# Optimization experiments

Hardware: AMD Instinct MI355X
Metric: run time of the kernel (lower is better)

Reference implementation:

```python
import jax, jax.numpy as jnp
import numpy as np

B, A, C, H, S, NR = 128, 2048, 128, 512, 3, 2
PR = C + 3 + S   # 134 read params per head
PW = 3 * C + 3 + S  # 390 write params


def setup_inputs() -> dict:
    key = jax.random.key(0)
    ks = jax.random.split(key, 8)
    h = jax.random.normal(ks[0], (B, H), jnp.float32)
    mem = jax.random.normal(ks[1], (B, A, C), jnp.float32)
    ra = jax.random.uniform(ks[2], (NR, B, A), jnp.float32)
    ra = ra / ra.sum(-1, keepdims=True)  # valid attention distributions
    wa = jax.random.uniform(ks[3], (B, A), jnp.float32)
    wa = wa / wa.sum(-1, keepdims=True)
    W_read = 0.02 * jax.random.normal(ks[4], (NR, PR, H), jnp.float32)
    b_read = jnp.zeros((NR, PR), jnp.float32)
    W_write = 0.02 * jax.random.normal(ks[5], (PW, H), jnp.float32)
    b_write = jnp.zeros((PW,), jnp.float32)
    return dict(h=h, mem=mem, prev_read_attn=ra, prev_write_attn=wa,
                W_read=W_read, b_read=b_read, W_write=W_write, b_write=b_write)


def _addressing(query, beta, gate, shift, gamma, mem, prev_w):
    """NTM addressing. query [...,C] (raw), beta/gate/gamma [...,1], shift [...,S],
    mem [B,A,C] (broadcasts), prev_w [...,A]. Returns attention [...,A]."""
    eps = 1e-8
    q = jax.nn.sigmoid(query)
    beta = jax.nn.softplus(beta) + 1.0
    gate = jax.nn.sigmoid(gate)
    shift_w = jax.nn.softmax(shift, axis=-1)
    gamma = jax.nn.softplus(gamma) + 1.0
    # content-based addressing: cosine similarity + sharpened softmax over A
    qn = jnp.maximum(jnp.linalg.norm(q, axis=-1, keepdims=True), eps)      # [...,1]
    mn = jnp.maximum(jnp.linalg.norm(mem, axis=-1), eps)                   # [B,A]
    sim = jnp.einsum('...c,...ac->...a', q, mem) / (qn * mn)
    w_c = jax.nn.softmax(beta * sim, axis=-1)
    # gated interpolation with previous attention
    w_g = gate * w_c + (1.0 - gate) * prev_w
    # circular shift convolution, offsets -(S//2)..S//2
    K = S // 2
    idx = (jnp.arange(A)[:, None] - (jnp.arange(S)[None, :] - K)) % A      # [A,S]
    w_s = jnp.einsum('...as,...s->...a', w_g[..., idx], shift_w)
    # gamma sharpening
    w_pow = w_s ** gamma
    return w_pow / (w_pow.sum(-1, keepdims=True) + 1e-12)


def reference(h, mem, prev_read_attn, prev_write_attn, W_read, b_read, W_write, b_write):
    # --- read heads (vectorized over NR heads) ---
    pr = jnp.einsum('bh,rph->rbp', h, W_read) + b_read[:, None, :]         # [NR,B,PR]
    q, beta, gate, shift, gamma = jnp.split(pr, [C, C + 1, C + 2, C + 2 + S], axis=-1)
    read_w = _addressing(q, beta, gate, shift, gamma, mem, prev_read_attn)  # [NR,B,A]
    read_vectors = jnp.einsum('rba,bac->rbc', read_w, mem)                 # [NR,B,C]
    # --- write head ---
    pw = h @ W_write.T + b_write                                           # [B,PW]
    locs = np.cumsum([C, 1, 1, S, 1, C])
    qw, bw, gw, sw, gmw, erase, add = jnp.split(pw, locs.tolist(), axis=-1)
    write_w = _addressing(qw, bw, gw, sw, gmw, mem, prev_write_attn)       # [B,A]
    e = jax.nn.sigmoid(erase)[:, None, :]                                  # [B,1,C]
    a = jax.nn.sigmoid(add)[:, None, :]                                    # [B,1,C]
    w = write_w[..., None]                                                 # [B,A,1]
    new_mem = mem * (1.0 - w * e) + w * a
    return read_vectors, new_mem
```

## Files before the change

kernel.cpp:

```cpp
#include <hip/hip_runtime.h>
#include <math.h>

constexpr int B_  = 128;
constexpr int A_  = 2048;
constexpr int C_  = 128;
constexpr int H_  = 512;
constexpr int S_  = 3;
constexpr int NR_ = 2;
constexpr int PR_ = C_ + 3 + S_;
constexpr int PW_ = 3 * C_ + 3 + S_;

typedef float vfloat4 __attribute__((ext_vector_type(4)));

__device__ __forceinline__ float sigmoidf_(float x) { return 1.0f / (1.0f + expf(-x)); }
__device__ __forceinline__ float softplusf_(float x) {
  return fmaxf(x, 0.0f) + log1pf(expf(-fabsf(x)));
}

__device__ __forceinline__ float waveReduceSum(float v) {
#pragma unroll
  for (int off = 32; off; off >>= 1) v += __shfl_xor(v, off, 64);
  return v;
}
__device__ __forceinline__ float waveReduceMax(float v) {
#pragma unroll
  for (int off = 32; off; off >>= 1) v = fmaxf(v, __shfl_xor(v, off, 64));
  return v;
}

__global__ __launch_bounds__(256) void proj_kernel(
    const float* __restrict__ h, const float* __restrict__ Wr,
    const float* __restrict__ br, const float* __restrict__ Ww,
    const float* __restrict__ bw, float* __restrict__ pr, float* __restrict__ pw) {
  constexpr int NPR = NR_ * B_ * PR_;
  constexpr int NPW = B_ * PW_;
  int wave = (blockIdx.x * blockDim.x + threadIdx.x) >> 6;
  int lane = threadIdx.x & 63;
  int out0 = wave * 2;
  const float* w0row;
  const float* w1row;
  const float* hrow;
  float bias0, bias1;
  float* outp;
  if (out0 < NPR) {
    int r = out0 / (B_ * PR_);
    int rem = out0 - r * (B_ * PR_);
    int b = rem / PR_;
    int p = rem - b * PR_;
    w0row = Wr + (size_t)(r * PR_ + p) * H_;
    w1row = w0row + H_;
    hrow = h + (size_t)b * H_;
    bias0 = br[r * PR_ + p];
    bias1 = br[r * PR_ + p + 1];
    outp = pr + out0;
  } else {
    int w2 = out0 - NPR;
    if (w2 >= NPW) return;
    int b = w2 / PW_;
    int p = w2 - b * PW_;
    w0row = Ww + (size_t)p * H_;
    w1row = w0row + H_;
    hrow = h + (size_t)b * H_;
    bias0 = bw[p];
    bias1 = bw[p + 1];
    outp = pw + w2;
  }
  const float4* h4 = (const float4*)hrow;
  const float4* wa4 = (const float4*)w0row;
  const float4* wb4 = (const float4*)w1row;
  float4 a0 = h4[(lane << 1)];
  float4 a1 = h4[(lane << 1) + 1];
  float4 b0 = wa4[(lane << 1)];
  float4 b1 = wa4[(lane << 1) + 1];
  float4 c0 = wb4[(lane << 1)];
  float4 c1 = wb4[(lane << 1) + 1];
  float acc0 = a0.x * b0.x;
  acc0 = fmaf(a0.y, b0.y, acc0);
  acc0 = fmaf(a0.z, b0.z, acc0);
  acc0 = fmaf(a0.w, b0.w, acc0);
  acc0 = fmaf(a1.x, b1.x, acc0);
  acc0 = fmaf(a1.y, b1.y, acc0);
  acc0 = fmaf(a1.z, b1.z, acc0);
  acc0 = fmaf(a1.w, b1.w, acc0);
  float acc1 = a0.x * c0.x;
  acc1 = fmaf(a0.y, c0.y, acc1);
  acc1 = fmaf(a0.z, c0.z, acc1);
  acc1 = fmaf(a0.w, c0.w, acc1);
  acc1 = fmaf(a1.x, c1.x, acc1);
  acc1 = fmaf(a1.y, c1.y, acc1);
  acc1 = fmaf(a1.z, c1.z, acc1);
  acc1 = fmaf(a1.w, c1.w, acc1);
  acc0 = waveReduceSum(acc0);
  acc1 = waveReduceSum(acc1);
  if (lane == 0) {
    outp[0] = acc0 + bias0;
    outp[1] = acc1 + bias1;
  }
}

__global__ __launch_bounds__(1024) void mega_kernel(
    const float* __restrict__ mem, const float* __restrict__ ra,
    const float* __restrict__ wa, const float* __restrict__ pr,
    const float* __restrict__ pw, float* __restrict__ rv,
    float* __restrict__ nmem) {
  __shared__ float sims[3][A_];
  __shared__ float wg[A_];
  __shared__ __align__(16) float qs[3 * C_];
  __shared__ float iqn[3];
  __shared__ float rbuf[16];
  __shared__ float4 red[2][16][32];

  int b = blockIdx.x;
  int tid = threadIdx.x;
  int lane = tid & 63;
  int wv = tid >> 6;

  if (tid < 3 * C_) {
    int hd = tid >> 7;
    int c = tid & (C_ - 1);
    float raw = (hd < 2) ? pr[(size_t)(hd * B_ + b) * PR_ + c]
                         : pw[(size_t)b * PW_ + c];
    qs[tid] = sigmoidf_(raw);
  }
  __syncthreads();
  if (wv < 3) {
    float v0 = qs[wv * C_ + lane];
    float v1 = qs[wv * C_ + 64 + lane];
    float ss = v0 * v0 + v1 * v1;
    ss = waveReduceSum(ss);
    if (lane == 0) iqn[wv] = 1.0f / fmaxf(sqrtf(ss), 1e-8f);
  }
  __syncthreads();

  {
    int j = tid & 7;
    int rgrp = tid >> 3;
    float4 q0[4], q1[4], q2[4];
    const float4* qs4 = (const float4*)qs;
#pragma unroll
    for (int k = 0; k < 4; k++) {
      q0[k] = qs4[j + 8 * k];
      q1[k] = qs4[32 + j + 8 * k];
      q2[k] = qs4[64 + j + 8 * k];
    }
    float iq0 = iqn[0], iq1 = iqn[1], iq2 = iqn[2];
#pragma unroll 2
    for (int i = 0; i < 16; i++) {
      int row = (i << 7) + rgrp;
      const float4* mrow = (const float4*)(mem + ((size_t)b * A_ + row) * C_);
      float d0 = 0.f, d1 = 0.f, d2 = 0.f, ss = 0.f;
#pragma unroll
      for (int k = 0; k < 4; k++) {
        float4 m = mrow[j + 8 * k];
        d0 = fmaf(m.x, q0[k].x, d0); d0 = fmaf(m.y, q0[k].y, d0);
        d0 = fmaf(m.z, q0[k].z, d0); d0 = fmaf(m.w, q0[k].w, d0);
        d1 = fmaf(m.x, q1[k].x, d1); d1 = fmaf(m.y, q1[k].y, d1);
        d1 = fmaf(m.z, q1[k].z, d1); d1 = fmaf(m.w, q1[k].w, d1);
        d2 = fmaf(m.x, q2[k].x, d2); d2 = fmaf(m.y, q2[k].y, d2);
        d2 = fmaf(m.z, q2[k].z, d2); d2 = fmaf(m.w, q2[k].w, d2);
        ss = fmaf(m.x, m.x, ss); ss = fmaf(m.y, m.y, ss);
        ss = fmaf(m.z, m.z, ss); ss = fmaf(m.w, m.w, ss);
      }
#pragma unroll
      for (int off = 1; off <= 4; off <<= 1) {
        d0 += __shfl_xor(d0, off, 64);
        d1 += __shfl_xor(d1, off, 64);
        d2 += __shfl_xor(d2, off, 64);
        ss += __shfl_xor(ss, off, 64);
      }
      if (j == 0) {
        float imn = 1.0f / fmaxf(sqrtf(ss), 1e-8f);
        sims[0][row] = d0 * iq0 * imn;
        sims[1][row] = d1 * iq1 * imn;
        sims[2][row] = d2 * iq2 * imn;
      }
    }
  }
  __syncthreads();

  for (int hd = 0; hd < 3; hd++) {
    const float* src = (hd < 2) ? (pr + (size_t)(hd * B_ + b) * PR_)
                                : (pw + (size_t)b * PW_);
    float braw = src[C_];
    float graw = src[C_ + 1];
    float s0r = src[C_ + 2], s1r = src[C_ + 3], s2r = src[C_ + 4];
    float gmraw = src[C_ + 5];
    float mx3 = fmaxf(s0r, fmaxf(s1r, s2r));
    float e0 = expf(s0r - mx3), e1 = expf(s1r - mx3), e2 = expf(s2r - mx3);
    float sinv = 1.0f / (e0 + e1 + e2);
    float beta = softplusf_(braw) + 1.0f;
    float gate = sigmoidf_(graw);
    float sw0 = e0 * sinv, sw1 = e1 * sinv, sw2 = e2 * sinv;
    float gamma = softplusf_(gmraw) + 1.0f;
    const float* prev = (hd < 2) ? (ra + (size_t)(hd * B_ + b) * A_)
                                 : (wa + (size_t)b * A_);

    float s0 = sims[hd][tid];
    float s1 = sims[hd][tid + 1024];
    float pv0 = prev[tid];
    float pv1 = prev[tid + 1024];

    float mx = fmaxf(s0, s1);
    mx = waveReduceMax(mx);
    if (lane == 0) rbuf[wv] = mx;
    __syncthreads();
    float M = rbuf[0];
#pragma unroll
    for (int i = 1; i < 16; i++) M = fmaxf(M, rbuf[i]);
    __syncthreads();

    float p0 = expf(beta * (s0 - M));
    float p1 = expf(beta * (s1 - M));
    float l = p0 + p1;
    l = waveReduceSum(l);
    if (lane == 0) rbuf[wv] = l;
    __syncthreads();
    float T = rbuf[0];
#pragma unroll
    for (int i = 1; i < 16; i++) T += rbuf[i];
    float inv = 1.0f / T;

    wg[tid] = fmaf(gate, p0 * inv, (1.0f - gate) * pv0);
    wg[tid + 1024] = fmaf(gate, p1 * inv, (1.0f - gate) * pv1);
    __syncthreads();

    float ws0 = sw0 * wg[(tid + 1) & (A_ - 1)] + sw1 * wg[tid] +
                sw2 * wg[(tid - 1) & (A_ - 1)];
    float ws1 = sw0 * wg[(tid + 1025) & (A_ - 1)] + sw1 * wg[tid + 1024] +
                sw2 * wg[(tid + 1023) & (A_ - 1)];
    float wp0 = (ws0 > 0.0f) ? exp2f(gamma * log2f(ws0)) : 0.0f;
    float wp1 = (ws1 > 0.0f) ? exp2f(gamma * log2f(ws1)) : 0.0f;
    float l2 = wp0 + wp1;
    l2 = waveReduceSum(l2);
    __syncthreads();
    if (lane == 0) rbuf[wv] = l2;
    __syncthreads();
    float T2 = rbuf[0];
#pragma unroll
    for (int i = 1; i < 16; i++) T2 += rbuf[i];
    float inv2 = 1.0f / (T2 + 1e-12f);
    sims[hd][tid] = wp0 * inv2;
    sims[hd][tid + 1024] = wp1 * inv2;
    __syncthreads();
  }

  {
    int quad = tid & 31;
    int rgrp = tid >> 5;
    int c0 = quad << 2;
    const float* pwrow = pw + (size_t)b * PW_;
    float2 eA = *(const float2*)(pwrow + C_ + 6 + c0);
    float2 eB = *(const float2*)(pwrow + C_ + 6 + c0 + 2);
    float2 aA = *(const float2*)(pwrow + 2 * C_ + 6 + c0);
    float2 aB = *(const float2*)(pwrow + 2 * C_ + 6 + c0 + 2);
    float e0 = sigmoidf_(eA.x), e1 = sigmoidf_(eA.y), e2 = sigmoidf_(eB.x), e3 = sigmoidf_(eB.y);
    float ad0 = sigmoidf_(aA.x), ad1 = sigmoidf_(aA.y), ad2 = sigmoidf_(aB.x), ad3 = sigmoidf_(aB.y);

    float4 acc0 = make_float4(0.f, 0.f, 0.f, 0.f);
    float4 acc1 = make_float4(0.f, 0.f, 0.f, 0.f);

#pragma unroll 4
    for (int i = 0; i < 64; i++) {
      int row = (i << 5) + rgrp;
      size_t base = ((size_t)b * A_ + row) * C_ + c0;
      float4 m = *(const float4*)(mem + base);
      float w0 = sims[0][row];
      float w1 = sims[1][row];
      float ww = sims[2][row];
      acc0.x = fmaf(w0, m.x, acc0.x);
      acc0.y = fmaf(w0, m.y, acc0.y);
      acc0.z = fmaf(w0, m.z, acc0.z);
      acc0.w = fmaf(w0, m.w, acc0.w);
      acc1.x = fmaf(w1, m.x, acc1.x);
      acc1.y = fmaf(w1, m.y, acc1.y);
      acc1.z = fmaf(w1, m.z, acc1.z);
      acc1.w = fmaf(w1, m.w, acc1.w);
      vfloat4 nm;
      nm.x = fmaf(m.x, 1.0f - ww * e0, ww * ad0);
      nm.y = fmaf(m.y, 1.0f - ww * e1, ww * ad1);
      nm.z = fmaf(m.z, 1.0f - ww * e2, ww * ad2);
      nm.w = fmaf(m.w, 1.0f - ww * e3, ww * ad3);
      __builtin_nontemporal_store(nm, (vfloat4*)(nmem + base));
    }

    acc0.x += __shfl_xor(acc0.x, 32, 64);
    acc0.y += __shfl_xor(acc0.y, 32, 64);
    acc0.z += __shfl_xor(acc0.z, 32, 64);
    acc0.w += __shfl_xor(acc0.w, 32, 64);
    acc1.x += __shfl_xor(acc1.x, 32, 64);
    acc1.y += __shfl_xor(acc1.y, 32, 64);
    acc1.z += __shfl_xor(acc1.z, 32, 64);
    acc1.w += __shfl_xor(acc1.w, 32, 64);
    if (lane < 32) {
      red[0][wv][lane] = acc0;
      red[1][wv][lane] = acc1;
    }
    __syncthreads();
    if (tid < 64) {
      int hd = tid >> 5;
      int q = tid & 31;
      float4 r = red[hd][0][q];
#pragma unroll
      for (int g = 1; g < 16; g++) {
        float4 t = red[hd][g][q];
        r.x += t.x; r.y += t.y; r.z += t.z; r.w += t.w;
      }
      float* rvp = rv + (size_t)(hd * B_ + b) * C_ + (q << 2);
      rvp[0] = r.x;
      rvp[1] = r.y;
      rvp[2] = r.z;
      rvp[3] = r.w;
    }
  }
}

extern "C" void kernel_launch(void* const* d_in, const int* in_sizes, int n_in,
                              void* d_out, int out_size, void* d_ws, size_t ws_size,
                              hipStream_t stream) {
  const float* h   = (const float*)d_in[0];
  const float* mem = (const float*)d_in[1];
  const float* ra  = (const float*)d_in[2];
  const float* wa  = (const float*)d_in[3];
  const float* Wr  = (const float*)d_in[4];
  const float* br  = (const float*)d_in[5];
  const float* Ww  = (const float*)d_in[6];
  const float* bw  = (const float*)d_in[7];

  float* out = (float*)d_out;
  float* rv = out;
  float* nmem = out + NR_ * B_ * C_;

  float* ws = (float*)d_ws;
  float* pr_buf = ws;
  float* pw_buf = pr_buf + NR_ * B_ * PR_;

  constexpr int NPAIRS = (NR_ * B_ * PR_ + B_ * PW_) / 2;
  proj_kernel<<<dim3(NPAIRS / 4), dim3(256), 0, stream>>>(h, Wr, br, Ww, bw, pr_buf, pw_buf);
  mega_kernel<<<dim3(B_), dim3(1024), 0, stream>>>(mem, ra, wa, pr_buf, pw_buf, rv, nmem);
}
```

Measured before the change: 293.0 us.

## Split each batch row across two cooperating workgroups with flag-based sim exchange

The main kernel now launches two workgroups per batch element, each computing cosine similarities for half of the memory rows. Each block publishes its half to a global buffer, and the pair waits on each other through release/acquire flags before both run the full addressing step. Each block then does the read and write pass over its own half, and the read vectors are combined with atomicAdd into an output that the projection kernel zeroes first. The aim is to go from 128 to 256 blocks so more of the GPU's CUs are busy, at the cost of a spin-wait that assumes both blocks of a pair are resident at the same time, plus extra global traffic.

New measurement: 309.1 us. 1.05x slower.

```diff
diff --git a/kernel.cpp b/kernel.cpp
--- a/kernel.cpp
+++ b/kernel.cpp
@@ -31,10 +31,14 @@
 __global__ __launch_bounds__(256) void proj_kernel(
     const float* __restrict__ h, const float* __restrict__ Wr,
     const float* __restrict__ br, const float* __restrict__ Ww,
-    const float* __restrict__ bw, float* __restrict__ pr, float* __restrict__ pw) {
+    const float* __restrict__ bw, float* __restrict__ pr, float* __restrict__ pw,
+    float* __restrict__ rv, int* __restrict__ flags) {
   constexpr int NPR = NR_ * B_ * PR_;
   constexpr int NPW = B_ * PW_;
-  int wave = (blockIdx.x * blockDim.x + threadIdx.x) >> 6;
+  int gid = blockIdx.x * blockDim.x + threadIdx.x;
+  if (gid < NR_ * B_ * C_) rv[gid] = 0.0f;
+  if (gid < 256) flags[gid] = 0;
+  int wave = gid >> 6;
   int lane = threadIdx.x & 63;
   int out0 = wave * 2;
   const float* w0row;
@@ -98,10 +102,11 @@
   }
 }
 
-__global__ __launch_bounds__(1024) void mega_kernel(
+__global__ __launch_bounds__(1024) void mega2_kernel(
     const float* __restrict__ mem, const float* __restrict__ ra,
     const float* __restrict__ wa, const float* __restrict__ pr,
-    const float* __restrict__ pw, float* __restrict__ rv,
+    const float* __restrict__ pw, float* __restrict__ simg,
+    int* __restrict__ flags, float* __restrict__ rv,
     float* __restrict__ nmem) {
   __shared__ float sims[3][A_];
   __shared__ float wg[A_];
@@ -110,7 +115,10 @@
   __shared__ float rbuf[16];
   __shared__ float4 red[2][16][32];
 
-  int b = blockIdx.x;
+  int bid = blockIdx.x;
+  int b = bid >> 1;
+  int half = bid & 1;
+  int rowbase = half << 10;
   int tid = threadIdx.x;
   int lane = tid & 63;
   int wv = tid >> 6;
@@ -145,8 +153,8 @@
     }
     float iq0 = iqn[0], iq1 = iqn[1], iq2 = iqn[2];
 #pragma unroll 2
-    for (int i = 0; i < 16; i++) {
-      int row = (i << 7) + rgrp;
+    for (int i = 0; i < 8; i++) {
+      int row = rowbase + (i << 7) + rgrp;
       const float4* mrow = (const float4*)(mem + ((size_t)b * A_ + row) * C_);
       float d0 = 0.f, d1 = 0.f, d2 = 0.f, ss = 0.f;
 #pragma unroll
@@ -170,10 +178,40 @@
       }
       if (j == 0) {
         float imn = 1.0f / fmaxf(sqrtf(ss), 1e-8f);
-        sims[0][row] = d0 * iq0 * imn;
-        sims[1][row] = d1 * iq1 * imn;
-        sims[2][row] = d2 * iq2 * imn;
+        float v0 = d0 * iq0 * imn;
+        float v1 = d1 * iq1 * imn;
+        float v2 = d2 * iq2 * imn;
+        sims[0][row] = v0;
+        sims[1][row] = v1;
+        sims[2][row] = v2;
+        __hip_atomic_store(&simg[(size_t)(0 * B_ + b) * A_ + row], v0,
+                           __ATOMIC_RELAXED, __HIP_MEMORY_SCOPE_AGENT);
+        __hip_atomic_store(&simg[(size_t)(1 * B_ + b) * A_ + row], v1,
+                           __ATOMIC_RELAXED, __HIP_MEMORY_SCOPE_AGENT);
+        __hip_atomic_store(&simg[(size_t)(2 * B_ + b) * A_ + row], v2,
+                           __ATOMIC_RELAXED, __HIP_MEMORY_SCOPE_AGENT);
       }
+    }
+  }
+  __syncthreads();
+
+  if (tid == 0) {
+    __hip_atomic_store(&flags[bid], 1, __ATOMIC_RELEASE, __HIP_MEMORY_SCOPE_AGENT);
+    while (__hip_atomic_load(&flags[bid ^ 1], __ATOMIC_ACQUIRE,
+                             __HIP_MEMORY_SCOPE_AGENT) == 0) {
+      __builtin_amdgcn_s_sleep(8);
+    }
+  }
+  __syncthreads();
+
+  {
+    int prow = (half ^ 1) << 10;
+    for (int idx = tid; idx < 3 * 1024; idx += 1024) {
+      int hd = idx >> 10;
+      int r = idx & 1023;
+      sims[hd][prow + r] =
+          __hip_atomic_load(&simg[(size_t)(hd * B_ + b) * A_ + prow + r],
+                            __ATOMIC_RELAXED, __HIP_MEMORY_SCOPE_AGENT);
     }
   }
   __syncthreads();
@@ -260,8 +298,8 @@
     float4 acc1 = make_float4(0.f, 0.f, 0.f, 0.f);
 
 #pragma unroll 4
-    for (int i = 0; i < 64; i++) {
-      int row = (i << 5) + rgrp;
+    for (int i = 0; i < 32; i++) {
+      int row = rowbase + (i << 5) + rgrp;
       size_t base = ((size_t)b * A_ + row) * C_ + c0;
       float4 m = *(const float4*)(mem + base);
       float w0 = sims[0][row];
@@ -306,10 +344,10 @@
         r.x += t.x; r.y += t.y; r.z += t.z; r.w += t.w;
       }
       float* rvp = rv + (size_t)(hd * B_ + b) * C_ + (q << 2);
-      rvp[0] = r.x;
-      rvp[1] = r.y;
-      rvp[2] = r.z;
-      rvp[3] = r.w;
+      atomicAdd(rvp + 0, r.x);
+      atomicAdd(rvp + 1, r.y);
+      atomicAdd(rvp + 2, r.z);
+      atomicAdd(rvp + 3, r.w);
     }
   }
 }
@@ -333,8 +371,12 @@
   float* ws = (float*)d_ws;
   float* pr_buf = ws;
   float* pw_buf = pr_buf + NR_ * B_ * PR_;
+  float* simg   = pw_buf + B_ * PW_;
+  int*   flags  = (int*)(simg + 3 * B_ * A_);
 
   constexpr int NPAIRS = (NR_ * B_ * PR_ + B_ * PW_) / 2;
-  proj_kernel<<<dim3(NPAIRS / 4), dim3(256), 0, stream>>>(h, Wr, br, Ww, bw, pr_buf, pw_buf);
-  mega_kernel<<<dim3(B_), dim3(1024), 0, stream>>>(mem, ra, wa, pr_buf, pw_buf, rv, nmem);
-}
+  proj_kernel<<<dim3(NPAIRS / 4), dim3(256), 0, stream>>>(h, Wr, br, Ww, bw,
+                                                          pr_buf, pw_buf, rv, flags);
+  mega2_kernel<<<dim3(2 * B_), dim3(1024), 0, stream>>>(mem, ra, wa, pr_buf,
+                                                        pw_buf, simg, flags, rv, nmem);
+}
```

## Fuse projection into main kernel and split read/write heads across block pairs

Applied to the files above, without the earlier changes.

Removes the separate projection kernel: each block computes its own head parameters from h and the weights into shared memory. The grid doubles to two blocks per batch row, with even blocks handling the two read heads and odd blocks handling the write head and new memory. This drops a launch and the workspace round-trip and gives 256 blocks instead of 128 to fill more CUs. In exchange, mem is now read by both blocks of each pair, and the weight matrices are re-read by every block.

New measurement: 303.7 us. 1.04x slower.

```diff
diff --git a/kernel.cpp b/kernel.cpp
--- a/kernel.cpp
+++ b/kernel.cpp
@@ -28,288 +28,402 @@
   return v;
 }
 
-__global__ __launch_bounds__(256) void proj_kernel(
-    const float* __restrict__ h, const float* __restrict__ Wr,
-    const float* __restrict__ br, const float* __restrict__ Ww,
-    const float* __restrict__ bw, float* __restrict__ pr, float* __restrict__ pw) {
-  constexpr int NPR = NR_ * B_ * PR_;
-  constexpr int NPW = B_ * PW_;
-  int wave = (blockIdx.x * blockDim.x + threadIdx.x) >> 6;
-  int lane = threadIdx.x & 63;
-  int out0 = wave * 2;
-  const float* w0row;
-  const float* w1row;
-  const float* hrow;
-  float bias0, bias1;
-  float* outp;
-  if (out0 < NPR) {
-    int r = out0 / (B_ * PR_);
-    int rem = out0 - r * (B_ * PR_);
-    int b = rem / PR_;
-    int p = rem - b * PR_;
-    w0row = Wr + (size_t)(r * PR_ + p) * H_;
-    w1row = w0row + H_;
-    hrow = h + (size_t)b * H_;
-    bias0 = br[r * PR_ + p];
-    bias1 = br[r * PR_ + p + 1];
-    outp = pr + out0;
-  } else {
-    int w2 = out0 - NPR;
-    if (w2 >= NPW) return;
-    int b = w2 / PW_;
-    int p = w2 - b * PW_;
-    w0row = Ww + (size_t)p * H_;
-    w1row = w0row + H_;
-    hrow = h + (size_t)b * H_;
-    bias0 = bw[p];
-    bias1 = bw[p + 1];
-    outp = pw + w2;
-  }
-  const float4* h4 = (const float4*)hrow;
-  const float4* wa4 = (const float4*)w0row;
-  const float4* wb4 = (const float4*)w1row;
-  float4 a0 = h4[(lane << 1)];
-  float4 a1 = h4[(lane << 1) + 1];
-  float4 b0 = wa4[(lane << 1)];
-  float4 b1 = wa4[(lane << 1) + 1];
-  float4 c0 = wb4[(lane << 1)];
-  float4 c1 = wb4[(lane << 1) + 1];
-  float acc0 = a0.x * b0.x;
-  acc0 = fmaf(a0.y, b0.y, acc0);
-  acc0 = fmaf(a0.z, b0.z, acc0);
-  acc0 = fmaf(a0.w, b0.w, acc0);
-  acc0 = fmaf(a1.x, b1.x, acc0);
-  acc0 = fmaf(a1.y, b1.y, acc0);
-  acc0 = fmaf(a1.z, b1.z, acc0);
-  acc0 = fmaf(a1.w, b1.w, acc0);
-  float acc1 = a0.x * c0.x;
-  acc1 = fmaf(a0.y, c0.y, acc1);
-  acc1 = fmaf(a0.z, c0.z, acc1);
-  acc1 = fmaf(a0.w, c0.w, acc1);
-  acc1 = fmaf(a1.x, c1.x, acc1);
-  acc1 = fmaf(a1.y, c1.y, acc1);
-  acc1 = fmaf(a1.z, c1.z, acc1);
-  acc1 = fmaf(a1.w, c1.w, acc1);
-  acc0 = waveReduceSum(acc0);
-  acc1 = waveReduceSum(acc1);
-  if (lane == 0) {
-    outp[0] = acc0 + bias0;
-    outp[1] = acc1 + bias1;
-  }
-}
-
-__global__ __launch_bounds__(1024) void mega_kernel(
-    const float* __restrict__ mem, const float* __restrict__ ra,
-    const float* __restrict__ wa, const float* __restrict__ pr,
-    const float* __restrict__ pw, float* __restrict__ rv,
-    float* __restrict__ nmem) {
-  __shared__ float sims[3][A_];
-  __shared__ float wg[A_];
-  __shared__ __align__(16) float qs[3 * C_];
-  __shared__ float iqn[3];
-  __shared__ float rbuf[16];
-  __shared__ float4 red[2][16][32];
-
-  int b = blockIdx.x;
+__device__ __forceinline__ float dot8_(float4 a0, float4 a1, float4 b0, float4 b1) {
+  float acc = a0.x * b0.x;
+  acc = fmaf(a0.y, b0.y, acc);
+  acc = fmaf(a0.z, b0.z, acc);
+  acc = fmaf(a0.w, b0.w, acc);
+  acc = fmaf(a1.x, b1.x, acc);
+  acc = fmaf(a1.y, b1.y, acc);
+  acc = fmaf(a1.z, b1.z, acc);
+  acc = fmaf(a1.w, b1.w, acc);
+  return acc;
+}
+
+struct SmemR {
+  float4 red[2][16][32];
+  float sims[2][A_];
+  float wg[A_];
+  alignas(16) float praw[2 * PR_];
+  alignas(16) float qs[2][C_];
+  float iqn[2];
+  float rbuf[16];
+};
+struct SmemW {
+  alignas(16) float qs[C_];
+  float sims[A_];
+  float wg[A_];
+  float praw[PW_];
+  float iqn1;
+  float rbuf[16];
+};
+union __align__(16) Smem {
+  SmemR r;
+  SmemW w;
+};
+
+__global__ __launch_bounds__(1024) void fused_kernel(
+    const float* __restrict__ h, const float* __restrict__ mem,
+    const float* __restrict__ ra, const float* __restrict__ wa,
+    const float* __restrict__ Wr, const float* __restrict__ br,
+    const float* __restrict__ Ww, const float* __restrict__ bw,
+    float* __restrict__ rv, float* __restrict__ nmem) {
+  __shared__ Smem sm;
+
+  int bid = blockIdx.x;
+  int b = bid >> 1;
   int tid = threadIdx.x;
   int lane = tid & 63;
   int wv = tid >> 6;
 
-  if (tid < 3 * C_) {
-    int hd = tid >> 7;
-    int c = tid & (C_ - 1);
-    float raw = (hd < 2) ? pr[(size_t)(hd * B_ + b) * PR_ + c]
-                         : pw[(size_t)b * PW_ + c];
-    qs[tid] = sigmoidf_(raw);
-  }
-  __syncthreads();
-  if (wv < 3) {
-    float v0 = qs[wv * C_ + lane];
-    float v1 = qs[wv * C_ + 64 + lane];
-    float ss = v0 * v0 + v1 * v1;
-    ss = waveReduceSum(ss);
-    if (lane == 0) iqn[wv] = 1.0f / fmaxf(sqrtf(ss), 1e-8f);
-  }
-  __syncthreads();
-
-  {
-    int j = tid & 7;
-    int rgrp = tid >> 3;
-    float4 q0[4], q1[4], q2[4];
-    const float4* qs4 = (const float4*)qs;
-#pragma unroll
-    for (int k = 0; k < 4; k++) {
-      q0[k] = qs4[j + 8 * k];
-      q1[k] = qs4[32 + j + 8 * k];
-      q2[k] = qs4[64 + j + 8 * k];
-    }
-    float iq0 = iqn[0], iq1 = iqn[1], iq2 = iqn[2];
+  const float4* h4 = (const float4*)(h + (size_t)b * H_);
+  float4 a0 = h4[lane << 1];
+  float4 a1 = h4[(lane << 1) + 1];
+
+  if ((bid & 1) == 0) {
+#pragma unroll
+    for (int pass = 0; pass < 9; ++pass) {
+      int out0 = pass * 32 + (wv << 1);
+      if (out0 < 2 * PR_) {
+        int hd = out0 >= PR_;
+        int p = out0 - hd * PR_;
+        const float4* w04 = (const float4*)(Wr + (size_t)(hd * PR_ + p) * H_);
+        const float4* w14 = (const float4*)(Wr + (size_t)(hd * PR_ + p + 1) * H_);
+        float4 b0 = w04[lane << 1];
+        float4 b1 = w04[(lane << 1) + 1];
+        float4 c0 = w14[lane << 1];
+        float4 c1 = w14[(lane << 1) + 1];
+        float acc0 = waveReduceSum(dot8_(a0, a1, b0, b1));
+        float acc1 = waveReduceSum(dot8_(a0, a1, c0, c1));
+        if (lane == 0) {
+          sm.r.praw[out0] = acc0 + br[hd * PR_ + p];
+          sm.r.praw[out0 + 1] = acc1 + br[hd * PR_ + p + 1];
+        }
+      }
+    }
+    __syncthreads();
+
+    if (tid < 2 * C_) {
+      int hd = tid >> 7;
+      int c = tid & (C_ - 1);
+      sm.r.qs[hd][c] = sigmoidf_(sm.r.praw[hd * PR_ + c]);
+    }
+    __syncthreads();
+    if (wv < 2) {
+      float v0 = sm.r.qs[wv][lane];
+      float v1 = sm.r.qs[wv][64 + lane];
+      float ss = waveReduceSum(v0 * v0 + v1 * v1);
+      if (lane == 0) sm.r.iqn[wv] = 1.0f / fmaxf(sqrtf(ss), 1e-8f);
+    }
+    __syncthreads();
+
+    {
+      int j = tid & 7;
+      int rgrp = tid >> 3;
+      float4 q0[4], q1[4];
+      const float4* q04 = (const float4*)sm.r.qs[0];
+      const float4* q14 = (const float4*)sm.r.qs[1];
+#pragma unroll
+      for (int k = 0; k < 4; k++) {
+        q0[k] = q04[j + 8 * k];
+        q1[k] = q14[j + 8 * k];
+      }
+      float iq0 = sm.r.iqn[0], iq1 = sm.r.iqn[1];
 #pragma unroll 2
-    for (int i = 0; i < 16; i++) {
-      int row = (i << 7) + rgrp;
-      const float4* mrow = (const float4*)(mem + ((size_t)b * A_ + row) * C_);
-      float d0 = 0.f, d1 = 0.f, d2 = 0.f, ss = 0.f;
-#pragma unroll
-      for (int k = 0; k < 4; k++) {
-        float4 m = mrow[j + 8 * k];
-        d0 = fmaf(m.x, q0[k].x, d0); d0 = fmaf(m.y, q0[k].y, d0);
-        d0 = fmaf(m.z, q0[k].z, d0); d0 = fmaf(m.w, q0[k].w, d0);
-        d1 = fmaf(m.x, q1[k].x, d1); d1 = fmaf(m.y, q1[k].y, d1);
-        d1 = fmaf(m.z, q1[k].z, d1); d1 = fmaf(m.w, q1[k].w, d1);
-        d2 = fmaf(m.x, q2[k].x, d2); d2 = fmaf(m.y, q2[k].y, d2);
-        d2 = fmaf(m.z, q2[k].z, d2); d2 = fmaf(m.w, q2[k].w, d2);
-        ss = fmaf(m.x, m.x, ss); ss = fmaf(m.y, m.y, ss);
-        ss = fmaf(m.z, m.z, ss); ss = fmaf(m.w, m.w, ss);
-      }
-#pragma unroll
-      for (int off = 1; off <= 4; off <<= 1) {
-        d0 += __shfl_xor(d0, off, 64);
-        d1 += __shfl_xor(d1, off, 64);
-        d2 += __shfl_xor(d2, off, 64);
-        ss += __shfl_xor(ss, off, 64);
-      }
-      if (j == 0) {
-        float imn = 1.0f / fmaxf(sqrtf(ss), 1e-8f);
-        sims[0][row] = d0 * iq0 * imn;
-        sims[1][row] = d1 * iq1 * imn;
-        sims[2][row] = d2 * iq2 * imn;
-      }
-    }
-  }
-  __syncthreads();
-
-  for (int hd = 0; hd < 3; hd++) {
-    const float* src = (hd < 2) ? (pr + (size_t)(hd * B_ + b) * PR_)
-                                : (pw + (size_t)b * PW_);
-    float braw = src[C_];
-    float graw = src[C_ + 1];
-    float s0r = src[C_ + 2], s1r = src[C_ + 3], s2r = src[C_ + 4];
-    float gmraw = src[C_ + 5];
-    float mx3 = fmaxf(s0r, fmaxf(s1r, s2r));
-    float e0 = expf(s0r - mx3), e1 = expf(s1r - mx3), e2 = expf(s2r - mx3);
-    float sinv = 1.0f / (e0 + e1 + e2);
-    float beta = softplusf_(braw) + 1.0f;
-    float gate = sigmoidf_(graw);
-    float sw0 = e0 * sinv, sw1 = e1 * sinv, sw2 = e2 * sinv;
-    float gamma = softplusf_(gmraw) + 1.0f;
-    const float* prev = (hd < 2) ? (ra + (size_t)(hd * B_ + b) * A_)
-                                 : (wa + (size_t)b * A_);
-
-    float s0 = sims[hd][tid];
-    float s1 = sims[hd][tid + 1024];
-    float pv0 = prev[tid];
-    float pv1 = prev[tid + 1024];
-
-    float mx = fmaxf(s0, s1);
-    mx = waveReduceMax(mx);
-    if (lane == 0) rbuf[wv] = mx;
-    __syncthreads();
-    float M = rbuf[0];
-#pragma unroll
-    for (int i = 1; i < 16; i++) M = fmaxf(M, rbuf[i]);
-    __syncthreads();
-
-    float p0 = expf(beta * (s0 - M));
-    float p1 = expf(beta * (s1 - M));
-    float l = p0 + p1;
-    l = waveReduceSum(l);
-    if (lane == 0) rbuf[wv] = l;
-    __syncthreads();
-    float T = rbuf[0];
-#pragma unroll
-    for (int i = 1; i < 16; i++) T += rbuf[i];
-    float inv = 1.0f / T;
-
-    wg[tid] = fmaf(gate, p0 * inv, (1.0f - gate) * pv0);
-    wg[tid + 1024] = fmaf(gate, p1 * inv, (1.0f - gate) * pv1);
-    __syncthreads();
-
-    float ws0 = sw0 * wg[(tid + 1) & (A_ - 1)] + sw1 * wg[tid] +
-                sw2 * wg[(tid - 1) & (A_ - 1)];
-    float ws1 = sw0 * wg[(tid + 1025) & (A_ - 1)] + sw1 * wg[tid + 1024] +
-                sw2 * wg[(tid + 1023) & (A_ - 1)];
-    float wp0 = (ws0 > 0.0f) ? exp2f(gamma * log2f(ws0)) : 0.0f;
-    float wp1 = (ws1 > 0.0f) ? exp2f(gamma * log2f(ws1)) : 0.0f;
-    float l2 = wp0 + wp1;
-    l2 = waveReduceSum(l2);
-    __syncthreads();
-    if (lane == 0) rbuf[wv] = l2;
-    __syncthreads();
-    float T2 = rbuf[0];
-#pragma unroll
-    for (int i = 1; i < 16; i++) T2 += rbuf[i];
-    float inv2 = 1.0f / (T2 + 1e-12f);
-    sims[hd][tid] = wp0 * inv2;
-    sims[hd][tid + 1024] = wp1 * inv2;
-    __syncthreads();
-  }
-
-  {
-    int quad = tid & 31;
-    int rgrp = tid >> 5;
-    int c0 = quad << 2;
-    const float* pwrow = pw + (size_t)b * PW_;
-    float2 eA = *(const float2*)(pwrow + C_ + 6 + c0);
-    float2 eB = *(const float2*)(pwrow + C_ + 6 + c0 + 2);
-    float2 aA = *(const float2*)(pwrow + 2 * C_ + 6 + c0);
-    float2 aB = *(const float2*)(pwrow + 2 * C_ + 6 + c0 + 2);
-    float e0 = sigmoidf_(eA.x), e1 = sigmoidf_(eA.y), e2 = sigmoidf_(eB.x), e3 = sigmoidf_(eB.y);
-    float ad0 = sigmoidf_(aA.x), ad1 = sigmoidf_(aA.y), ad2 = sigmoidf_(aB.x), ad3 = sigmoidf_(aB.y);
-
-    float4 acc0 = make_float4(0.f, 0.f, 0.f, 0.f);
-    float4 acc1 = make_float4(0.f, 0.f, 0.f, 0.f);
-
+      for (int i = 0; i < 16; i++) {
+        int row = (i << 7) + rgrp;
+        const float4* mrow = (const float4*)(mem + ((size_t)b * A_ + row) * C_);
+        float d0 = 0.f, d1 = 0.f, ss = 0.f;
+#pragma unroll
+        for (int k = 0; k < 4; k++) {
+          float4 m = mrow[j + 8 * k];
+          d0 = fmaf(m.x, q0[k].x, d0); d0 = fmaf(m.y, q0[k].y, d0);
+          d0 = fmaf(m.z, q0[k].z, d0); d0 = fmaf(m.w, q0[k].w, d0);
+          d1 = fmaf(m.x, q1[k].x, d1); d1 = fmaf(m.y, q1[k].y, d1);
+          d1 = fmaf(m.z, q1[k].z, d1); d1 = fmaf(m.w, q1[k].w, d1);
+          ss = fmaf(m.x, m.x, ss); ss = fmaf(m.y, m.y, ss);
+          ss = fmaf(m.z, m.z, ss); ss = fmaf(m.w, m.w, ss);
+        }
+#pragma unroll
+        for (int off = 1; off <= 4; off <<= 1) {
+          d0 += __shfl_xor(d0, off, 64);
+          d1 += __shfl_xor(d1, off, 64);
+          ss += __shfl_xor(ss, off, 64);
+        }
+        if (j == 0) {
+          float imn = 1.0f / fmaxf(sqrtf(ss), 1e-8f);
+          sm.r.sims[0][row] = d0 * iq0 * imn;
+          sm.r.sims[1][row] = d1 * iq1 * imn;
+        }
+      }
+    }
+    __syncthreads();
+
+    for (int hd = 0; hd < 2; hd++) {
+      float braw = sm.r.praw[hd * PR_ + C_];
+      float graw = sm.r.praw[hd * PR_ + C_ + 1];
+      float s0r = sm.r.praw[hd * PR_ + C_ + 2];
+      float s1r = sm.r.praw[hd * PR_ + C_ + 3];
+      float s2r = sm.r.praw[hd * PR_ + C_ + 4];
+      float gmraw = sm.r.praw[hd * PR_ + C_ + 5];
+      float mx3 = fmaxf(s0r, fmaxf(s1r, s2r));
+      float e0 = expf(s0r - mx3), e1 = expf(s1r - mx3), e2 = expf(s2r - mx3);
+      float sinv = 1.0f / (e0 + e1 + e2);
+      float beta = softplusf_(braw) + 1.0f;
+      float gate = sigmoidf_(graw);
+      float sw0 = e0 * sinv, sw1 = e1 * sinv, sw2 = e2 * sinv;
+      float gamma = softplusf_(gmraw) + 1.0f;
+      const float* prev = ra + (size_t)(hd * B_ + b) * A_;
+
+      float s0 = sm.r.sims[hd][tid];
+      float s1 = sm.r.sims[hd][tid + 1024];
+      float pv0 = prev[tid];
+      float pv1 = prev[tid + 1024];
+
+      float mx = waveReduceMax(fmaxf(s0, s1));
+      if (lane == 0) sm.r.rbuf[wv] = mx;
+      __syncthreads();
+      float M = sm.r.rbuf[0];
+#pragma unroll
+      for (int i = 1; i < 16; i++) M = fmaxf(M, sm.r.rbuf[i]);
+      __syncthreads();
+
+      float p0 = expf(beta * (s0 - M));
+      float p1 = expf(beta * (s1 - M));
+      float l = waveReduceSum(p0 + p1);
+      if (lane == 0) sm.r.rbuf[wv] = l;
+      __syncthreads();
+      float T = sm.r.rbuf[0];
+#pragma unroll
+      for (int i = 1; i < 16; i++) T += sm.r.rbuf[i];
+      float inv = 1.0f / T;
+
+      sm.r.wg[tid] = fmaf(gate, p0 * inv, (1.0f - gate) * pv0);
+      sm.r.wg[tid + 1024] = fmaf(gate, p1 * inv, (1.0f - gate) * pv1);
+      __syncthreads();
+
+      float ws0 = sw0 * sm.r.wg[(tid + 1) & (A_ - 1)] + sw1 * sm.r.wg[tid] +
+                  sw2 * sm.r.wg[(tid - 1) & (A_ - 1)];
+      float ws1 = sw0 * sm.r.wg[(tid + 1025) & (A_ - 1)] + sw1 * sm.r.wg[tid + 1024] +
+                  sw2 * sm.r.wg[(tid + 1023) & (A_ - 1)];
+      float wp0 = (ws0 > 0.0f) ? exp2f(gamma * log2f(ws0)) : 0.0f;
+      float wp1 = (ws1 > 0.0f) ? exp2f(gamma * log2f(ws1)) : 0.0f;
+      float l2 = waveReduceSum(wp0 + wp1);
+      __syncthreads();
+      if (lane == 0) sm.r.rbuf[wv] = l2;
+      __syncthreads();
+      float T2 = sm.r.rbuf[0];
+#pragma unroll
+      for (int i = 1; i < 16; i++) T2 += sm.r.rbuf[i];
+      float inv2 = 1.0f / (T2 + 1e-12f);
+      sm.r.sims[hd][tid] = wp0 * inv2;
+      sm.r.sims[hd][tid + 1024] = wp1 * inv2;
+      __syncthreads();
+    }
+
+    {
+      int quad = tid & 31;
+      int rgrp = tid >> 5;
+      int c0 = quad << 2;
+      float4 acc0 = make_float4(0.f, 0.f, 0.f, 0.f);
+      float4 acc1 = make_float4(0.f, 0.f, 0.f, 0.f);
 #pragma unroll 4
-    for (int i = 0; i < 64; i++) {
-      int row = (i << 5) + rgrp;
-      size_t base = ((size_t)b * A_ + row) * C_ + c0;
-      float4 m = *(const float4*)(mem + base);
-      float w0 = sims[0][row];
-      float w1 = sims[1][row];
-      float ww = sims[2][row];
-      acc0.x = fmaf(w0, m.x, acc0.x);
-      acc0.y = fmaf(w0, m.y, acc0.y);
-      acc0.z = fmaf(w0, m.z, acc0.z);
-      acc0.w = fmaf(w0, m.w, acc0.w);
-      acc1.x = fmaf(w1, m.x, acc1.x);
-      acc1.y = fmaf(w1, m.y, acc1.y);
-      acc1.z = fmaf(w1, m.z, acc1.z);
-      acc1.w = fmaf(w1, m.w, acc1.w);
-      vfloat4 nm;
-      nm.x = fmaf(m.x, 1.0f - ww * e0, ww * ad0);
-      nm.y = fmaf(m.y, 1.0f - ww * e1, ww * ad1);
-      nm.z = fmaf(m.z, 1.0f - ww * e2, ww * ad2);
-      nm.w = fmaf(m.w, 1.0f - ww * e3, ww * ad3);
-      __builtin_nontemporal_store(nm, (vfloat4*)(nmem + base));
-    }
-
-    acc0.x += __shfl_xor(acc0.x, 32, 64);
-    acc0.y += __shfl_xor(acc0.y, 32, 64);
-    acc0.z += __shfl_xor(acc0.z, 32, 64);
-    acc0.w += __shfl_xor(acc0.w, 32, 64);
-    acc1.x += __shfl_xor(acc1.x, 32, 64);
-    acc1.y += __shfl_xor(acc1.y, 32, 64);
-    acc1.z += __shfl_xor(acc1.z, 32, 64);
-    acc1.w += __shfl_xor(acc1.w, 32, 64);
-    if (lane < 32) {
-      red[0][wv][lane] = acc0;
-      red[1][wv][lane] = acc1;
-    }
-    __syncthreads();
-    if (tid < 64) {
-      int hd = tid >> 5;
-      int q = tid & 31;
-      float4 r = red[hd][0][q];
-#pragma unroll
-      for (int g = 1; g < 16; g++) {
-        float4 t = red[hd][g][q];
-        r.x += t.x; r.y += t.y; r.z += t.z; r.w += t.w;
-      }
-      float* rvp = rv + (size_t)(hd * B_ + b) * C_ + (q << 2);
-      rvp[0] = r.x;
-      rvp[1] = r.y;
-      rvp[2] = r.z;
-      rvp[3] = r.w;
+      for (int i = 0; i < 64; i++) {
+        int row = (i << 5) + rgrp;
+        size_t base = ((size_t)b * A_ + row) * C_ + c0;
+        float4 m = *(const float4*)(mem + base);
+        float w0 = sm.r.sims[0][row];
+        float w1 = sm.r.sims[1][row];
+        acc0.x = fmaf(w0, m.x, acc0.x);
+        acc0.y = fmaf(w0, m.y, acc0.y);
+        acc0.z = fmaf(w0, m.z, acc0.z);
+        acc0.w = fmaf(w0, m.w, acc0.w);
+        acc1.x = fmaf(w1, m.x, acc1.x);
+        acc1.y = fmaf(w1, m.y, acc1.y);
+        acc1.z = fmaf(w1, m.z, acc1.z);
+        acc1.w = fmaf(w1, m.w, acc1.w);
+      }
+      acc0.x += __shfl_xor(acc0.x, 32, 64);
+      acc0.y += __shfl_xor(acc0.y, 32, 64);
+      acc0.z += __shfl_xor(acc0.z, 32, 64);
+      acc0.w += __shfl_xor(acc0.w, 32, 64);
+      acc1.x += __shfl_xor(acc1.x, 32, 64);
+      acc1.y += __shfl_xor(acc1.y, 32, 64);
+      acc1.z += __shfl_xor(acc1.z, 32, 64);
+      acc1.w += __shfl_xor(acc1.w, 32, 64);
+      if (lane < 32) {
+        sm.r.red[0][wv][lane] = acc0;
+        sm.r.red[1][wv][lane] = acc1;
+      }
+      __syncthreads();
+      if (tid < 64) {
+        int hd = tid >> 5;
+        int q = tid & 31;
+        float4 r = sm.r.red[hd][0][q];
+#pragma unroll
+        for (int g = 1; g < 16; g++) {
+          float4 t = sm.r.red[hd][g][q];
+          r.x += t.x; r.y += t.y; r.z += t.z; r.w += t.w;
+        }
+        float* rvp = rv + (size_t)(hd * B_ + b) * C_ + (q << 2);
+        rvp[0] = r.x;
+        rvp[1] = r.y;
+        rvp[2] = r.z;
+        rvp[3] = r.w;
+      }
+    }
+  } else {
+#pragma unroll
+    for (int pass = 0; pass < 13; ++pass) {
+      int out0 = pass * 32 + (wv << 1);
+      if (out0 < PW_) {
+        const float4* w04 = (const float4*)(Ww + (size_t)out0 * H_);
+        const float4* w14 = (const float4*)(Ww + (size_t)(out0 + 1) * H_);
+        float4 b0 = w04[lane << 1];
+        float4 b1 = w04[(lane << 1) + 1];
+        float4 c0 = w14[lane << 1];
+        float4 c1 = w14[(lane << 1) + 1];
+        float acc0 = waveReduceSum(dot8_(a0, a1, b0, b1));
+        float acc1 = waveReduceSum(dot8_(a0, a1, c0, c1));
+        if (lane == 0) {
+          sm.w.praw[out0] = acc0 + bw[out0];
+          sm.w.praw[out0 + 1] = acc1 + bw[out0 + 1];
+        }
+      }
+    }
+    __syncthreads();
+
+    if (tid < C_) sm.w.qs[tid] = sigmoidf_(sm.w.praw[tid]);
+    __syncthreads();
+    if (wv == 0) {
+      float v0 = sm.w.qs[lane];
+      float v1 = sm.w.qs[64 + lane];
+      float ss = waveReduceSum(v0 * v0 + v1 * v1);
+      if (lane == 0) sm.w.iqn1 = 1.0f / fmaxf(sqrtf(ss), 1e-8f);
+    }
+    __syncthreads();
+
+    {
+      int j = tid & 7;
+      int rgrp = tid >> 3;
+      float4 q2[4];
+      const float4* q24 = (const float4*)sm.w.qs;
+#pragma unroll
+      for (int k = 0; k < 4; k++) q2[k] = q24[j + 8 * k];
+      float iq2 = sm.w.iqn1;
+#pragma unroll 2
+      for (int i = 0; i < 16; i++) {
+        int row = (i << 7) + rgrp;
+        const float4* mrow = (const float4*)(mem + ((size_t)b * A_ + row) * C_);
+        float d2 = 0.f, ss = 0.f;
+#pragma unroll
+        for (int k = 0; k < 4; k++) {
+          float4 m = mrow[j + 8 * k];
+          d2 = fmaf(m.x, q2[k].x, d2); d2 = fmaf(m.y, q2[k].y, d2);
+          d2 = fmaf(m.z, q2[k].z, d2); d2 = fmaf(m.w, q2[k].w, d2);
+          ss = fmaf(m.x, m.x, ss); ss = fmaf(m.y, m.y, ss);
+          ss = fmaf(m.z, m.z, ss); ss = fmaf(m.w, m.w, ss);
+        }
+#pragma unroll
+        for (int off = 1; off <= 4; off <<= 1) {
+          d2 += __shfl_xor(d2, off, 64);
+          ss += __shfl_xor(ss, off, 64);
+        }
+        if (j == 0) {
+          float imn = 1.0f / fmaxf(sqrtf(ss), 1e-8f);
+          sm.w.sims[row] = d2 * iq2 * imn;
+        }
+      }
+    }
+    __syncthreads();
+
+    {
+      float braw = sm.w.praw[C_];
+      float graw = sm.w.praw[C_ + 1];
+      float s0r = sm.w.praw[C_ + 2];
+      float s1r = sm.w.praw[C_ + 3];
+      float s2r = sm.w.praw[C_ + 4];
+      float gmraw = sm.w.praw[C_ + 5];
+      float mx3 = fmaxf(s0r, fmaxf(s1r, s2r));
+      float e0 = expf(s0r - mx3), e1 = expf(s1r - mx3), e2 = expf(s2r - mx3);
+      float sinv = 1.0f / (e0 + e1 + e2);
+      float beta = softplusf_(braw) + 1.0f;
+      float gate = sigmoidf_(graw);
+      float sw0 = e0 * sinv, sw1 = e1 * sinv, sw2 = e2 * sinv;
+      float gamma = softplusf_(gmraw) + 1.0f;
+      const float* prev = wa + (size_t)b * A_;
+
+      float s0 = sm.w.sims[tid];
+      float s1 = sm.w.sims[tid + 1024];
+      float pv0 = prev[tid];
+      float pv1 = prev[tid + 1024];
+
+      float mx = waveReduceMax(fmaxf(s0, s1));
+      if (lane == 0) sm.w.rbuf[wv] = mx;
+      __syncthreads();
+      float M = sm.w.rbuf[0];
+#pragma unroll
+      for (int i = 1; i < 16; i++) M = fmaxf(M, sm.w.rbuf[i]);
+      __syncthreads();
+
+      float p0 = expf(beta * (s0 - M));
+      float p1 = expf(beta * (s1 - M));
+      float l = waveReduceSum(p0 + p1);
+      if (lane == 0) sm.w.rbuf[wv] = l;
+      __syncthreads();
+      float T = sm.w.rbuf[0];
+#pragma unroll
+      for (int i = 1; i < 16; i++) T += sm.w.rbuf[i];
+      float inv = 1.0f / T;
+
+      sm.w.wg[tid] = fmaf(gate, p0 * inv, (1.0f - gate) * pv0);
+      sm.w.wg[tid + 1024] = fmaf(gate, p1 * inv, (1.0f - gate) * pv1);
+      __syncthreads();
+
+      float ws0 = sw0 * sm.w.wg[(tid + 1) & (A_ - 1)] + sw1 * sm.w.wg[tid] +
+                  sw2 * sm.w.wg[(tid - 1) & (A_ - 1)];
+      float ws1 = sw0 * sm.w.wg[(tid + 1025) & (A_ - 1)] + sw1 * sm.w.wg[tid + 1024] +
+                  sw2 * sm.w.wg[(tid + 1023) & (A_ - 1)];
+      float wp0 = (ws0 > 0.0f) ? exp2f(gamma * log2f(ws0)) : 0.0f;
+      float wp1 = (ws1 > 0.0f) ? exp2f(gamma * log2f(ws1)) : 0.0f;
+      float l2 = waveReduceSum(wp0 + wp1);
+      __syncthreads();
+      if (lane == 0) sm.w.rbuf[wv] = l2;
+      __syncthreads();
+      float T2 = sm.w.rbuf[0];
+#pragma unroll
+      for (int i = 1; i < 16; i++) T2 += sm.w.rbuf[i];
+      float inv2 = 1.0f / (T2 + 1e-12f);
+      sm.w.sims[tid] = wp0 * inv2;
+      sm.w.sims[tid + 1024] = wp1 * inv2;
+      __syncthreads();
+    }
+
+    {
+      int quad = tid & 31;
+      int rgrp = tid >> 5;
+      int c0 = quad << 2;
+      float e0 = sigmoidf_(sm.w.praw[C_ + 6 + c0]);
+      float e1 = sigmoidf_(sm.w.praw[C_ + 6 + c0 + 1]);
+      float e2 = sigmoidf_(sm.w.praw[C_ + 6 + c0 + 2]);
+      float e3 = sigmoidf_(sm.w.praw[C_ + 6 + c0 + 3]);
+      float ad0 = sigmoidf_(sm.w.praw[2 * C_ + 6 + c0]);
+      float ad1 = sigmoidf_(sm.w.praw[2 * C_ + 6 + c0 + 1]);
+      float ad2 = sigmoidf_(sm.w.praw[2 * C_ + 6 + c0 + 2]);
+      float ad3 = sigmoidf_(sm.w.praw[2 * C_ + 6 + c0 + 3]);
+#pragma unroll 4
+      for (int i = 0; i < 64; i++) {
+        int row = (i << 5) + rgrp;
+        size_t base = ((size_t)b * A_ + row) * C_ + c0;
+        float4 m = *(const float4*)(mem + base);
+        float ww = sm.w.sims[row];
+        vfloat4 nm;
+        nm.x = fmaf(m.x, 1.0f - ww * e0, ww * ad0);
+        nm.y = fmaf(m.y, 1.0f - ww * e1, ww * ad1);
+        nm.z = fmaf(m.z, 1.0f - ww * e2, ww * ad2);
+        nm.w = fmaf(m.w, 1.0f - ww * e3, ww * ad3);
+        __builtin_nontemporal_store(nm, (vfloat4*)(nmem + base));
+      }
     }
   }
 }
@@ -330,11 +444,6 @@
   float* rv = out;
   float* nmem = out + NR_ * B_ * C_;
 
-  float* ws = (float*)d_ws;
-  float* pr_buf = ws;
-  float* pw_buf = pr_buf + NR_ * B_ * PR_;
-
-  constexpr int NPAIRS = (NR_ * B_ * PR_ + B_ * PW_) / 2;
-  proj_kernel<<<dim3(NPAIRS / 4), dim3(256), 0, stream>>>(h, Wr, br, Ww, bw, pr_buf, pw_buf);
-  mega_kernel<<<dim3(B_), dim3(1024), 0, stream>>>(mem, ra, wa, pr_buf, pw_buf, rv, nmem);
-}
+  fused_kernel<<<dim3(2 * B_), dim3(1024), 0, stream>>>(h, mem, ra, wa, Wr, br,
+                                                        Ww, bw, rv, nmem);
+}
```

## Split mega kernel into sim and attention-update kernels over half-row blocks

Applied to the files above, without the earlier changes.

Splits the single per-batch kernel into a similarity kernel and an attention/update kernel, each launched with two blocks per batch row that cover half of the A dimension. This doubles the grid from 128 to 256 blocks so more CUs are used. The cost is an extra global round trip for the similarity scores, an extra launch, and the softmax/shift work being done redundantly by both halves. Read vectors are now combined with atomicAdd into an output that the projection kernel zeroes first.

After: 297.3 us. No clear change (+1.5%).

```diff
diff --git a/kernel.cpp b/kernel.cpp
--- a/kernel.cpp
+++ b/kernel.cpp
@@ -31,10 +31,13 @@
 __global__ __launch_bounds__(256) void proj_kernel(
     const float* __restrict__ h, const float* __restrict__ Wr,
     const float* __restrict__ br, const float* __restrict__ Ww,
-    const float* __restrict__ bw, float* __restrict__ pr, float* __restrict__ pw) {
+    const float* __restrict__ bw, float* __restrict__ pr, float* __restrict__ pw,
+    float* __restrict__ rv) {
   constexpr int NPR = NR_ * B_ * PR_;
   constexpr int NPW = B_ * PW_;
-  int wave = (blockIdx.x * blockDim.x + threadIdx.x) >> 6;
+  int gid = blockIdx.x * blockDim.x + threadIdx.x;
+  if (gid < NR_ * B_ * C_) rv[gid] = 0.0f;
+  int wave = gid >> 6;
   int lane = threadIdx.x & 63;
   int out0 = wave * 2;
   const float* w0row;
@@ -98,19 +101,15 @@
   }
 }
 
-__global__ __launch_bounds__(1024) void mega_kernel(
-    const float* __restrict__ mem, const float* __restrict__ ra,
-    const float* __restrict__ wa, const float* __restrict__ pr,
-    const float* __restrict__ pw, float* __restrict__ rv,
-    float* __restrict__ nmem) {
-  __shared__ float sims[3][A_];
-  __shared__ float wg[A_];
+__global__ __launch_bounds__(1024) void sim_half_kernel(
+    const float* __restrict__ mem, const float* __restrict__ pr,
+    const float* __restrict__ pw, float* __restrict__ simg) {
   __shared__ __align__(16) float qs[3 * C_];
   __shared__ float iqn[3];
-  __shared__ float rbuf[16];
-  __shared__ float4 red[2][16][32];
-
-  int b = blockIdx.x;
+
+  int bid = blockIdx.x;
+  int b = bid >> 1;
+  int rowbase = (bid & 1) << 10;
   int tid = threadIdx.x;
   int lane = tid & 63;
   int wv = tid >> 6;
@@ -126,55 +125,79 @@
   if (wv < 3) {
     float v0 = qs[wv * C_ + lane];
     float v1 = qs[wv * C_ + 64 + lane];
-    float ss = v0 * v0 + v1 * v1;
-    ss = waveReduceSum(ss);
+    float ss = waveReduceSum(v0 * v0 + v1 * v1);
     if (lane == 0) iqn[wv] = 1.0f / fmaxf(sqrtf(ss), 1e-8f);
   }
   __syncthreads();
 
-  {
-    int j = tid & 7;
-    int rgrp = tid >> 3;
-    float4 q0[4], q1[4], q2[4];
-    const float4* qs4 = (const float4*)qs;
+  int j = tid & 7;
+  int rgrp = tid >> 3;
+  float4 q0[4], q1[4], q2[4];
+  const float4* qs4 = (const float4*)qs;
+#pragma unroll
+  for (int k = 0; k < 4; k++) {
+    q0[k] = qs4[j + 8 * k];
+    q1[k] = qs4[32 + j + 8 * k];
+    q2[k] = qs4[64 + j + 8 * k];
+  }
+  float iq0 = iqn[0], iq1 = iqn[1], iq2 = iqn[2];
+
+#pragma unroll 2
+  for (int i = 0; i < 8; i++) {
+    int row = rowbase + (i << 7) + rgrp;
+    const float4* mrow = (const float4*)(mem + ((size_t)b * A_ + row) * C_);
+    float d0 = 0.f, d1 = 0.f, d2 = 0.f, ss = 0.f;
 #pragma unroll
     for (int k = 0; k < 4; k++) {
-      q0[k] = qs4[j + 8 * k];
-      q1[k] = qs4[32 + j + 8 * k];
-      q2[k] = qs4[64 + j + 8 * k];
-    }
-    float iq0 = iqn[0], iq1 = iqn[1], iq2 = iqn[2];
-#pragma unroll 2
-    for (int i = 0; i < 16; i++) {
-      int row = (i << 7) + rgrp;
-      const float4* mrow = (const float4*)(mem + ((size_t)b * A_ + row) * C_);
-      float d0 = 0.f, d1 = 0.f, d2 = 0.f, ss = 0.f;
-#pragma unroll
-      for (int k = 0; k < 4; k++) {
-        float4 m = mrow[j + 8 * k];
-        d0 = fmaf(m.x, q0[k].x, d0); d0 = fmaf(m.y, q0[k].y, d0);
-        d0 = fmaf(m.z, q0[k].z, d0); d0 = fmaf(m.w, q0[k].w, d0);
-        d1 = fmaf(m.x, q1[k].x, d1); d1 = fmaf(m.y, q1[k].y, d1);
-        d1 = fmaf(m.z, q1[k].z, d1); d1 = fmaf(m.w, q1[k].w, d1);
-        d2 = fmaf(m.x, q2[k].x, d2); d2 = fmaf(m.y, q2[k].y, d2);
-        d2 = fmaf(m.z, q2[k].z, d2); d2 = fmaf(m.w, q2[k].w, d2);
-        ss = fmaf(m.x, m.x, ss); ss = fmaf(m.y, m.y, ss);
-        ss = fmaf(m.z, m.z, ss); ss = fmaf(m.w, m.w, ss);
-      }
-#pragma unroll
-      for (int off = 1; off <= 4; off <<= 1) {
-        d0 += __shfl_xor(d0, off, 64);
-        d1 += __shfl_xor(d1, off, 64);
-        d2 += __shfl_xor(d2, off, 64);
-        ss += __shfl_xor(ss, off, 64);
-      }
-      if (j == 0) {
-        float imn = 1.0f / fmaxf(sqrtf(ss), 1e-8f);
-        sims[0][row] = d0 * iq0 * imn;
-        sims[1][row] = d1 * iq1 * imn;
-        sims[2][row] = d2 * iq2 * imn;
-      }
-    }
+      float4 m = mrow[j + 8 * k];
+      d0 = fmaf(m.x, q0[k].x, d0); d0 = fmaf(m.y, q0[k].y, d0);
+      d0 = fmaf(m.z, q0[k].z, d0); d0 = fmaf(m.w, q0[k].w, d0);
+      d1 = fmaf(m.x, q1[k].x, d1); d1 = fmaf(m.y, q1[k].y, d1);
+      d1 = fmaf(m.z, q1[k].z, d1); d1 = fmaf(m.w, q1[k].w, d1);
+      d2 = fmaf(m.x, q2[k].x, d2); d2 = fmaf(m.y, q2[k].y, d2);
+      d2 = fmaf(m.z, q2[k].z, d2); d2 = fmaf(m.w, q2[k].w, d2);
+      ss = fmaf(m.x, m.x, ss); ss = fmaf(m.y, m.y, ss);
+      ss = fmaf(m.z, m.z, ss); ss = fmaf(m.w, m.w, ss);
+    }
+#pragma unroll
+    for (int off = 1; off <= 4; off <<= 1) {
+      d0 += __shfl_xor(d0, off, 64);
+      d1 += __shfl_xor(d1, off, 64);
+      d2 += __shfl_xor(d2, off, 64);
+      ss += __shfl_xor(ss, off, 64);
+    }
+    if (j == 0) {
+      float imn = 1.0f / fmaxf(sqrtf(ss), 1e-8f);
+      simg[(size_t)(0 * B_ + b) * A_ + row] = d0 * iq0 * imn;
+      simg[(size_t)(1 * B_ + b) * A_ + row] = d1 * iq1 * imn;
+      simg[(size_t)(2 * B_ + b) * A_ + row] = d2 * iq2 * imn;
+    }
+  }
+}
+
+__global__ __launch_bounds__(1024) void attn_update_kernel(
+    const float* __restrict__ mem, const float* __restrict__ ra,
+    const float* __restrict__ wa, const float* __restrict__ pr,
+    const float* __restrict__ pw, const float* __restrict__ simg,
+    float* __restrict__ rv, float* __restrict__ nmem) {
+  __shared__ float sims[3][A_];
+  __shared__ float wg[A_];
+  __shared__ float rbuf[16];
+  __shared__ float4 red[2][16][32];
+
+  int bid = blockIdx.x;
+  int b = bid >> 1;
+  int rowbase = (bid & 1) << 10;
+  int tid = threadIdx.x;
+  int lane = tid & 63;
+  int wv = tid >> 6;
+
+#pragma unroll
+  for (int k = 0; k < 6; k++) {
+    int idx = k * 1024 + tid;
+    int hd = idx >> 11;
+    int r = idx & (A_ - 1);
+    sims[hd][r] = simg[(size_t)(hd * B_ + b) * A_ + r];
   }
   __syncthreads();
 
@@ -200,8 +223,7 @@
     float pv0 = prev[tid];
     float pv1 = prev[tid + 1024];
 
-    float mx = fmaxf(s0, s1);
-    mx = waveReduceMax(mx);
+    float mx = waveReduceMax(fmaxf(s0, s1));
     if (lane == 0) rbuf[wv] = mx;
     __syncthreads();
     float M = rbuf[0];
@@ -211,8 +233,7 @@
 
     float p0 = expf(beta * (s0 - M));
     float p1 = expf(beta * (s1 - M));
-    float l = p0 + p1;
-    l = waveReduceSum(l);
+    float l = waveReduceSum(p0 + p1);
     if (lane == 0) rbuf[wv] = l;
     __syncthreads();
     float T = rbuf[0];
@@ -230,8 +251,7 @@
                 sw2 * wg[(tid + 1023) & (A_ - 1)];
     float wp0 = (ws0 > 0.0f) ? exp2f(gamma * log2f(ws0)) : 0.0f;
     float wp1 = (ws1 > 0.0f) ? exp2f(gamma * log2f(ws1)) : 0.0f;
-    float l2 = wp0 + wp1;
-    l2 = waveReduceSum(l2);
+    float l2 = waveReduceSum(wp0 + wp1);
     __syncthreads();
     if (lane == 0) rbuf[wv] = l2;
     __syncthreads();
@@ -260,8 +280,8 @@
     float4 acc1 = make_float4(0.f, 0.f, 0.f, 0.f);
 
 #pragma unroll 4
-    for (int i = 0; i < 64; i++) {
-      int row = (i << 5) + rgrp;
+    for (int i = 0; i < 32; i++) {
+      int row = rowbase + (i << 5) + rgrp;
       size_t base = ((size_t)b * A_ + row) * C_ + c0;
       float4 m = *(const float4*)(mem + base);
       float w0 = sims[0][row];
@@ -306,10 +326,10 @@
         r.x += t.x; r.y += t.y; r.z += t.z; r.w += t.w;
       }
       float* rvp = rv + (size_t)(hd * B_ + b) * C_ + (q << 2);
-      rvp[0] = r.x;
-      rvp[1] = r.y;
-      rvp[2] = r.z;
-      rvp[3] = r.w;
+      atomicAdd(rvp + 0, r.x);
+      atomicAdd(rvp + 1, r.y);
+      atomicAdd(rvp + 2, r.z);
+      atomicAdd(rvp + 3, r.w);
     }
   }
 }
@@ -333,8 +353,12 @@
   float* ws = (float*)d_ws;
   float* pr_buf = ws;
   float* pw_buf = pr_buf + NR_ * B_ * PR_;
+  float* simg   = pw_buf + B_ * PW_;
 
   constexpr int NPAIRS = (NR_ * B_ * PR_ + B_ * PW_) / 2;
-  proj_kernel<<<dim3(NPAIRS / 4), dim3(256), 0, stream>>>(h, Wr, br, Ww, bw, pr_buf, pw_buf);
-  mega_kernel<<<dim3(B_), dim3(1024), 0, stream>>>(mem, ra, wa, pr_buf, pw_buf, rv, nmem);
-}
+  proj_kernel<<<dim3(NPAIRS / 4), dim3(256), 0, stream>>>(h, Wr, br, Ww, bw,
+                                                          pr_buf, pw_buf, rv);
+  sim_half_kernel<<<dim3(2 * B_), dim3(1024), 0, stream>>>(mem, pr_buf, pw_buf, simg);
+  attn_update_kernel<<<dim3(2 * B_), dim3(1024), 0, stream>>>(mem, ra, wa, pr_buf,
+                                                              pw_buf, simg, rv, nmem);
+}
```
